# Kernel tuning notes

Measured on AMD Instinct MI355X. Metric: run time of the kernel, lower is better.

## Reference

```python
import math
import jax, jax.numpy as jnp
import numpy as np

NLAT, NLON = 61, 120
C, H = 64, 4
DH = C // H
HID = 128
NSEG = NLAT * NLON  # number of grid points / softmax segments
EPS = 1e-6
SCALE = 1.0 / math.sqrt(DH)


def _build_geometry():
    """Neighbor pairs within theta_cutoff on the equiangular (pole-including) grid.

    The neighborhood structure is longitude-shift invariant, so we enumerate it
    for output longitude 0 and replicate with a modular longitude shift.
    """
    nlat, nlon = NLAT, NLON
    theta = np.pi * np.arange(nlat) / (nlat - 1)           # colatitudes incl. poles
    lam = 2.0 * np.pi * np.arange(nlon) / nlon
    theta_cutoff = 7.0 / math.sqrt(math.pi) * math.pi / (nlat - 1)
    ct, st = np.cos(theta), np.sin(theta)
    # great-circle distance between (theta_o, 0) and (theta_i, dlon): [nlat, nlat, nlon]
    cosd = (ct[:, None, None] * ct[None, :, None]
            + st[:, None, None] * st[None, :, None] * np.cos(lam)[None, None, :])
    dist = np.arccos(np.clip(cosd, -1.0, 1.0))
    ho, hi, dl = np.nonzero(dist <= theta_cutoff)          # E reference-column entries
    wo = np.arange(nlon)
    out_idx = (ho[:, None] * nlon + wo[None, :]).reshape(-1).astype(np.int32)
    in_idx = (hi[:, None] * nlon + (dl[:, None] + wo[None, :]) % nlon).reshape(-1).astype(np.int32)
    # quadrature (integration) weights: sin(theta) measure, zero at the poles
    w = (st * (np.pi / (nlat - 1)) * (2.0 * np.pi / nlon)).astype(np.float32)
    quad_w = np.repeat(w, nlon)                            # [NSEG]
    return jnp.asarray(out_idx), jnp.asarray(in_idx), jnp.asarray(quad_w)


def setup_inputs() -> dict:
    key = jax.random.key(0)
    ks = jax.random.split(key, 8)
    out_idx, in_idx, quad_w = _build_geometry()

    def w(k, shape, fan_in):
        return jax.random.normal(k, shape, dtype=jnp.float32) / np.float32(np.sqrt(fan_in))

    return {
        "x": jax.random.normal(ks[0], (1, C, NLAT, NLON), dtype=jnp.float32),
        "wq": w(ks[1], (C, C), C),
        "wk": w(ks[2], (C, C), C),
        "wv": w(ks[3], (C, C), C),
        "wo": w(ks[4], (C, C), C),
        "w1": w(ks[5], (HID, C), C),
        "b1": jnp.zeros((HID,), jnp.float32),
        "w2": w(ks[6], (C, HID), HID),
        "b2": jnp.zeros((C,), jnp.float32),
        "ln0_g": jnp.ones((C,), jnp.float32),
        "ln0_b": jnp.zeros((C,), jnp.float32),
        "ln1_g": jnp.ones((C,), jnp.float32),
        "ln1_b": jnp.zeros((C,), jnp.float32),
        "quad_w": quad_w,
        "out_idx": out_idx,
        "in_idx": in_idx,
    }


def _layernorm(x, g, b):
    # channel-wise LayerNorm at every spatial location; x: [B, C, H, W]
    m = jnp.mean(x, axis=1, keepdims=True)
    v = jnp.mean((x - m) ** 2, axis=1, keepdims=True)
    xh = (x - m) * jax.lax.rsqrt(v + EPS)
    return xh * g[None, :, None, None] + b[None, :, None, None]


def _neighborhood_attn(x, wq, wk, wv, wo, quad_w, out_idx, in_idx):
    # x: [B, C, nlat, nlon] (fp32)
    B = x.shape[0]
    q = jnp.einsum('oc,bchw->bohw', wq, x).reshape(B, H, DH, NSEG)
    k = jnp.einsum('oc,bchw->bohw', wk, x).reshape(B, H, DH, NSEG)
    v = jnp.einsum('oc,bchw->bohw', wv, x).reshape(B, H, DH, NSEG)
    qg = q[..., out_idx]                                   # [B,H,DH,NNZ]
    kg = k[..., in_idx]
    s = jnp.einsum('bhdn,bhdn->bhn', qg, kg) * SCALE       # [B,H,NNZ]
    s = jnp.moveaxis(s, -1, 0)                             # [NNZ,B,H]
    smax = jax.ops.segment_max(s, out_idx, num_segments=NSEG)
    # quadrature-weighted, numerically stable softmax over each neighborhood
    alpha = jnp.exp(s - smax[out_idx]) * quad_w[in_idx][:, None, None]
    vg = jnp.moveaxis(v[..., in_idx], -1, 0)               # [NNZ,B,H,DH]
    num = jax.ops.segment_sum(alpha[..., None] * vg, out_idx, num_segments=NSEG)
    den = jax.ops.segment_sum(alpha, out_idx, num_segments=NSEG)
    att = num / den[..., None]                             # [NSEG,B,H,DH]
    att = jnp.moveaxis(att, 0, -1).reshape(B, C, NLAT, NLON)
    return jnp.einsum('oc,bchw->bohw', wo, att)


def reference(x, wq, wk, wv, wo, w1, b1, w2, b2, ln0_g, ln0_b, ln1_g, ln1_b,
              quad_w, out_idx, in_idx):
    residual = x
    h0 = _layernorm(x, ln0_g, ln0_b)
    a = _neighborhood_attn(h0.astype(jnp.float32), wq, wk, wv, wo,
                           quad_w, out_idx, in_idx).astype(x.dtype)
    x1 = a + residual
    h1 = _layernorm(x1, ln1_g, ln1_b)
    m = jax.nn.gelu(jnp.einsum('fc,bchw->bfhw', w1, h1) + b1[None, :, None, None],
                    approximate=False)
    m = jnp.einsum('cf,bfhw->bchw', w2, m) + b2[None, :, None, None]
    return m + x1
```

## Files before the change

kernel.cpp:

```cpp
#include <hip/hip_runtime.h>
#include <math.h>

#define NSEG 7320
#define NLON 120
#define HIDN 128
#define ECH  16
#define MAXCH 48

__global__ __launch_bounds__(64) void k1_ln_qkv(
    const float* __restrict__ x,  const float* __restrict__ wq,
    const float* __restrict__ wk, const float* __restrict__ wv,
    const float* __restrict__ g,  const float* __restrict__ b,
    const int* __restrict__ out_idx, const int* __restrict__ in_idx,
    const float* __restrict__ qw, int E,
    float* __restrict__ q_pl, float* __restrict__ k_pl, float* __restrict__ v_pl,
    int* __restrict__ row_start, int4* __restrict__ meta,
    float4* __restrict__ zbase)
{
    const int lane = threadIdx.x;
    const int tile = blockIdx.x;
    const int grp  = blockIdx.y;

    if (grp >= 25) {
        const int n4 = (68 * NSEG) / 4;
        for (int i = ((grp - 25) * 115 + tile) * 64 + lane; i < n4; i += 2 * 115 * 64)
            zbase[i] = make_float4(0.f, 0.f, 0.f, 0.f);
        return;
    }
    if (grp == 24) {
        for (int e = tile * 64 + lane; e < E; e += 115 * 64) {
            int ho = out_idx[e * NLON] / NLON;
            if (e == 0) {
                row_start[ho] = 0;
            } else {
                int hp = out_idx[(e - 1) * NLON] / NLON;
                if (hp != ho) row_start[ho] = e;
            }
            if (e == E - 1) row_start[ho + 1] = E;
            int i0 = in_idx[e * NLON];
            int hi = i0 / NLON;
            int dl = i0 - hi * NLON;
            meta[e] = make_int4(hi * NLON, dl, __float_as_int(qw[i0]), ho);
        }
        return;
    }

    const int n = tile * 64 + lane;
    if (n >= NSEG) return;

    float xv[64];
    float s = 0.f, s2 = 0.f;
#pragma unroll
    for (int c = 0; c < 64; ++c) { float t = x[c * NSEG + n]; xv[c] = t; s += t; s2 += t * t; }
    float mean = s * 0.015625f;
    float var  = s2 * 0.015625f - mean * mean;
    float rstd = rsqrtf(var + 1e-6f);
#pragma unroll
    for (int c = 0; c < 64; ++c) xv[c] = (xv[c] - mean) * rstd * g[c] + b[c];

    const int mm    = grp >> 3;
    const int obase = (grp & 7) * 8;
    const float* __restrict__ w = (mm == 0) ? wq : (mm == 1) ? wk : wv;
    float* __restrict__ dst = (mm == 0) ? q_pl : (mm == 1) ? k_pl : v_pl;
    const float scale = (mm == 0) ? 0.25f : 1.0f;

#pragma unroll
    for (int j = 0; j < 8; ++j) {
        int o = obase + j;
        float acc = 0.f;
#pragma unroll
        for (int c = 0; c < 64; ++c) acc += w[o * 64 + c] * xv[c];
        dst[o * NSEG + n] = acc * scale;
    }
}

__global__ __launch_bounds__(128) void k2_attn(
    const float* __restrict__ q_pl, const float* __restrict__ k_pl,
    const float* __restrict__ v_pl,
    const int4* __restrict__ meta,  const int* __restrict__ row_start,
    float* __restrict__ num, float* __restrict__ den)
{
    const int wo  = threadIdx.x;
    const bool aw = wo < NLON;
    const int woc = aw ? wo : (NLON - 1);
    const int ho  = blockIdx.x;
    const int head = blockIdx.z;
    const int cb  = head * 16;

    int e0 = __builtin_amdgcn_readfirstlane(row_start[ho]);
    int e1 = __builtin_amdgcn_readfirstlane(row_start[ho + 1]);
    int eb = e0 + blockIdx.y * ECH;
    if (eb >= e1) return;
    int ee = eb + ECH; if (ee > e1) ee = e1;

    const int segc = ho * NLON + woc;
    const float* __restrict__ qb = q_pl + (size_t)cb * NSEG;
    const float* __restrict__ kb = k_pl + (size_t)cb * NSEG;
    const float* __restrict__ vb = v_pl + (size_t)cb * NSEG;

    float qreg[16];
#pragma unroll
    for (int c = 0; c < 16; ++c) qreg[c] = qb[c * NSEG + segc];

    float acc[16];
#pragma unroll
    for (int c = 0; c < 16; ++c) acc[c] = 0.f;
    float dh = 0.f;

#pragma unroll 2
    for (int e = eb; e < ee; ++e) {
        int4 mt = meta[e];
        int dlw = mt.y + woc; if (dlw >= NLON) dlw -= NLON;
        const float* __restrict__ kp = kb + (mt.x + dlw);
        const float* __restrict__ vp = vb + (mt.x + dlw);

        float sa = 0.f, sb = 0.f;
#pragma unroll
        for (int c = 0; c < 8; ++c)  sa += qreg[c]     * kp[c * NSEG];
#pragma unroll
        for (int c = 0; c < 8; ++c)  sb += qreg[8 + c] * kp[(8 + c) * NSEG];

        float qwv = aw ? __int_as_float(mt.z) : 0.f;
        float a = __expf(sa + sb) * qwv;
        dh += a;

#pragma unroll
        for (int c = 0; c < 16; ++c) acc[c] = fmaf(a, vp[c * NSEG], acc[c]);
    }

    if (aw) {
        const int seg = ho * NLON + wo;
#pragma unroll
        for (int c = 0; c < 16; ++c) atomicAdd(&num[(cb + c) * NSEG + seg], acc[c]);
        atomicAdd(&den[head * NSEG + seg], dh);
    }
}

__global__ __launch_bounds__(64) void k2c_wo(
    const float* __restrict__ num, const float* __restrict__ den,
    const float* __restrict__ wo,  const float* __restrict__ x,
    float* __restrict__ x1)
{
    const int lane = threadIdx.x;
    const int n    = blockIdx.x * 64 + lane;
    if (n >= NSEG) return;

    float rdh[4];
#pragma unroll
    for (int h = 0; h < 4; ++h) rdh[h] = 1.0f / den[h * NSEG + n];

    float att[64];
#pragma unroll
    for (int c = 0; c < 64; ++c) att[c] = num[c * NSEG + n] * rdh[c >> 4];

    const int o0 = blockIdx.y * 8;
#pragma unroll
    for (int j = 0; j < 8; ++j) {
        int o = o0 + j;
        float acc = 0.f;
#pragma unroll
        for (int c = 0; c < 64; ++c) acc += wo[o * 64 + c] * att[c];
        x1[o * NSEG + n] = acc + x[o * NSEG + n];
    }
}

__global__ __launch_bounds__(64) void k3a_mlp1(
    const float* __restrict__ x1, const float* __restrict__ w1,
    const float* __restrict__ b1, const float* __restrict__ g,
    const float* __restrict__ bb, float* __restrict__ m_act)
{
    const int lane = threadIdx.x;
    const int n    = blockIdx.x * 64 + lane;
    if (n >= NSEG) return;

    float xv[64];
    float s = 0.f, s2 = 0.f;
#pragma unroll
    for (int c = 0; c < 64; ++c) { float t = x1[c * NSEG + n]; xv[c] = t; s += t; s2 += t * t; }
    float mean = s * 0.015625f;
    float var  = s2 * 0.015625f - mean * mean;
    float rstd = rsqrtf(var + 1e-6f);
#pragma unroll
    for (int c = 0; c < 64; ++c) xv[c] = (xv[c] - mean) * rstd * g[c] + bb[c];

    const int h0 = blockIdx.y * 8;
#pragma unroll
    for (int j = 0; j < 8; ++j) {
        int h = h0 + j;
        float mh = b1[h];
#pragma unroll
        for (int c = 0; c < 64; ++c) mh += w1[h * 64 + c] * xv[c];
        m_act[h * NSEG + n] = 0.5f * mh * (1.0f + erff(mh * 0.70710678118654752f));
    }
}

__global__ __launch_bounds__(64) void k3b_mlp2(
    const float* __restrict__ m_act, const float* __restrict__ w2,
    const float* __restrict__ b2,    const float* __restrict__ x1,
    float* __restrict__ out)
{
    const int lane = threadIdx.x;
    const int n    = blockIdx.x * 64 + lane;
    if (n >= NSEG) return;
    const int c0   = blockIdx.y * 8;

    float acc[8];
#pragma unroll
    for (int j = 0; j < 8; ++j) acc[j] = 0.f;

#pragma unroll 8
    for (int h = 0; h < HIDN; ++h) {
        float mh = m_act[h * NSEG + n];
#pragma unroll
        for (int j = 0; j < 8; ++j) acc[j] += w2[(c0 + j) * HIDN + h] * mh;
    }
#pragma unroll
    for (int j = 0; j < 8; ++j) {
        int c = c0 + j;
        out[c * NSEG + n] = acc[j] + b2[c] + x1[c * NSEG + n];
    }
}

extern "C" void kernel_launch(void* const* d_in, const int* in_sizes, int n_in,
                              void* d_out, int out_size, void* d_ws, size_t ws_size,
                              hipStream_t stream)
{
    const float* x    = (const float*)d_in[0];
    const float* wq   = (const float*)d_in[1];
    const float* wk   = (const float*)d_in[2];
    const float* wv   = (const float*)d_in[3];
    const float* wo   = (const float*)d_in[4];
    const float* w1   = (const float*)d_in[5];
    const float* b1   = (const float*)d_in[6];
    const float* w2   = (const float*)d_in[7];
    const float* b2   = (const float*)d_in[8];
    const float* ln0g = (const float*)d_in[9];
    const float* ln0b = (const float*)d_in[10];
    const float* ln1g = (const float*)d_in[11];
    const float* ln1b = (const float*)d_in[12];
    const float* qw   = (const float*)d_in[13];
    const int* out_idx = (const int*)d_in[14];
    const int* in_idx  = (const int*)d_in[15];
    float* out = (float*)d_out;

    const int NNZ = in_sizes[15];
    const int E   = NNZ / NLON;
    const size_t N64 = (size_t)NSEG * 64;

    float* ws    = (float*)d_ws;
    float* q_pl  = ws;
    float* k_pl  = ws + N64;
    float* v_pl  = ws + 2 * N64;
    float* num   = ws + 3 * N64;
    float* den   = ws + 4 * N64;
    float* x1    = ws + 4 * N64 + 4 * NSEG;
    float* m_act = ws + 5 * N64 + 4 * NSEG;
    int*   row_start = (int*)(ws + 7 * N64 + 4 * NSEG);
    int4*  meta  = (int4*)(ws + 7 * N64 + 4 * NSEG + 64);

    hipLaunchKernelGGL(k1_ln_qkv, dim3(115, 27), dim3(64), 0, stream,
                       x, wq, wk, wv, ln0g, ln0b, out_idx, in_idx, qw, E,
                       q_pl, k_pl, v_pl, row_start, meta, (float4*)num);
    hipLaunchKernelGGL(k2_attn, dim3(61, MAXCH, 4), dim3(128), 0, stream,
                       q_pl, k_pl, v_pl, meta, row_start, num, den);
    hipLaunchKernelGGL(k2c_wo, dim3(115, 8), dim3(64), 0, stream,
                       num, den, wo, x, x1);
    hipLaunchKernelGGL(k3a_mlp1, dim3(115, 16), dim3(64), 0, stream,
                       x1, w1, b1, ln1g, ln1b, m_act);
    hipLaunchKernelGGL(k3b_mlp2, dim3(115, 8), dim3(64), 0, stream,
                       m_act, w2, b2, x1, out);
}
```

Measured before the change: 186.8 us.

## Fuse output projection with MLP first layer and flatten attention grid ordering

Merges the Wo projection plus residual kernel with the LayerNorm and first MLP layer kernel. Each block recomputes the full 64-channel x1 in registers, then produces 16 hidden units, and only the first y-block writes x1. This removes one launch and the x1 write-then-read round trip, but the Wo GEMV is now repeated 8 times per point and the larger register arrays may reduce occupancy. The attention kernel grid becomes a 1D launch where consecutive block IDs cover groups of 8 latitude rows for the same head and chunk, which changes scheduling and cache locality, and the id-to-row mapping skips rows at or above 61.

```diff
diff --git a/kernel.cpp b/kernel.cpp
--- a/kernel.cpp
+++ b/kernel.cpp
@@ -80,16 +80,20 @@
     const int4* __restrict__ meta,  const int* __restrict__ row_start,
     float* __restrict__ num, float* __restrict__ den)
 {
+    const int id   = blockIdx.x;
+    const int ho   = (id & 7) + 8 * ((id >> 3) & 7);
+    if (ho >= 61) return;
+    const int ch   = id >> 6;
+    const int head = ch & 3;
+    const int cb   = head * 16;
+
     const int wo  = threadIdx.x;
     const bool aw = wo < NLON;
     const int woc = aw ? wo : (NLON - 1);
-    const int ho  = blockIdx.x;
-    const int head = blockIdx.z;
-    const int cb  = head * 16;
 
     int e0 = __builtin_amdgcn_readfirstlane(row_start[ho]);
     int e1 = __builtin_amdgcn_readfirstlane(row_start[ho + 1]);
-    int eb = e0 + blockIdx.y * ECH;
+    int eb = e0 + (ch >> 2) * ECH;
     if (eb >= e1) return;
     int ee = eb + ECH; if (ee > e1) ee = e1;
 
@@ -136,10 +140,12 @@
     }
 }
 
-__global__ __launch_bounds__(64) void k2c_wo(
+__global__ __launch_bounds__(64) void k23a_wo_mlp1(
     const float* __restrict__ num, const float* __restrict__ den,
     const float* __restrict__ wo,  const float* __restrict__ x,
-    float* __restrict__ x1)
+    const float* __restrict__ w1,  const float* __restrict__ b1,
+    const float* __restrict__ g1,  const float* __restrict__ bb1,
+    float* __restrict__ x1, float* __restrict__ m_act)
 {
     const int lane = threadIdx.x;
     const int n    = blockIdx.x * 64 + lane;
@@ -149,49 +155,43 @@
 #pragma unroll
     for (int h = 0; h < 4; ++h) rdh[h] = 1.0f / den[h * NSEG + n];
 
-    float att[64];
-#pragma unroll
-    for (int c = 0; c < 64; ++c) att[c] = num[c * NSEG + n] * rdh[c >> 4];
-
-    const int o0 = blockIdx.y * 8;
-#pragma unroll
-    for (int j = 0; j < 8; ++j) {
-        int o = o0 + j;
-        float acc = 0.f;
-#pragma unroll
-        for (int c = 0; c < 64; ++c) acc += wo[o * 64 + c] * att[c];
-        x1[o * NSEG + n] = acc + x[o * NSEG + n];
-    }
-}
-
-__global__ __launch_bounds__(64) void k3a_mlp1(
-    const float* __restrict__ x1, const float* __restrict__ w1,
-    const float* __restrict__ b1, const float* __restrict__ g,
-    const float* __restrict__ bb, float* __restrict__ m_act)
-{
-    const int lane = threadIdx.x;
-    const int n    = blockIdx.x * 64 + lane;
-    if (n >= NSEG) return;
-
-    float xv[64];
+    float x1v[64];
+#pragma unroll
+    for (int o = 0; o < 64; ++o) x1v[o] = x[o * NSEG + n];
+
+    for (int c = 0; c < 64; ++c) {
+        float att = num[c * NSEG + n] * rdh[c >> 4];
+        const float* __restrict__ wcol = wo + c;
+#pragma unroll
+        for (int o = 0; o < 64; ++o) x1v[o] = fmaf(wcol[o * 64], att, x1v[o]);
+    }
+
+    if (blockIdx.y == 0) {
+#pragma unroll
+        for (int o = 0; o < 64; ++o) x1[o * NSEG + n] = x1v[o];
+    }
+
     float s = 0.f, s2 = 0.f;
 #pragma unroll
-    for (int c = 0; c < 64; ++c) { float t = x1[c * NSEG + n]; xv[c] = t; s += t; s2 += t * t; }
+    for (int o = 0; o < 64; ++o) { s += x1v[o]; s2 += x1v[o] * x1v[o]; }
     float mean = s * 0.015625f;
     float var  = s2 * 0.015625f - mean * mean;
     float rstd = rsqrtf(var + 1e-6f);
-#pragma unroll
-    for (int c = 0; c < 64; ++c) xv[c] = (xv[c] - mean) * rstd * g[c] + bb[c];
-
-    const int h0 = blockIdx.y * 8;
-#pragma unroll
-    for (int j = 0; j < 8; ++j) {
-        int h = h0 + j;
-        float mh = b1[h];
-#pragma unroll
-        for (int c = 0; c < 64; ++c) mh += w1[h * 64 + c] * xv[c];
-        m_act[h * NSEG + n] = 0.5f * mh * (1.0f + erff(mh * 0.70710678118654752f));
-    }
+
+    const int h0 = blockIdx.y * 16;
+    float mh[16];
+#pragma unroll
+    for (int j = 0; j < 16; ++j) mh[j] = b1[h0 + j];
+    for (int c = 0; c < 64; ++c) {
+        float xn = (x1v[c] - mean) * rstd * g1[c] + bb1[c];
+        const float* __restrict__ w1c = w1 + h0 * 64 + c;
+#pragma unroll
+        for (int j = 0; j < 16; ++j) mh[j] = fmaf(w1c[j * 64], xn, mh[j]);
+    }
+#pragma unroll
+    for (int j = 0; j < 16; ++j)
+        m_act[(h0 + j) * NSEG + n] =
+            0.5f * mh[j] * (1.0f + erff(mh[j] * 0.70710678118654752f));
 }
 
 __global__ __launch_bounds__(64) void k3b_mlp2(
@@ -261,12 +261,10 @@
     hipLaunchKernelGGL(k1_ln_qkv, dim3(115, 27), dim3(64), 0, stream,
                        x, wq, wk, wv, ln0g, ln0b, out_idx, in_idx, qw, E,
                        q_pl, k_pl, v_pl, row_start, meta, (float4*)num);
-    hipLaunchKernelGGL(k2_attn, dim3(61, MAXCH, 4), dim3(128), 0, stream,
+    hipLaunchKernelGGL(k2_attn, dim3(64 * 192), dim3(128), 0, stream,
                        q_pl, k_pl, v_pl, meta, row_start, num, den);
-    hipLaunchKernelGGL(k2c_wo, dim3(115, 8), dim3(64), 0, stream,
-                       num, den, wo, x, x1);
-    hipLaunchKernelGGL(k3a_mlp1, dim3(115, 16), dim3(64), 0, stream,
-                       x1, w1, b1, ln1g, ln1b, m_act);
+    hipLaunchKernelGGL(k23a_wo_mlp1, dim3(115, 8), dim3(64), 0, stream,
+                       num, den, wo, x, w1, b1, ln1g, ln1b, x1, m_act);
     hipLaunchKernelGGL(k3b_mlp2, dim3(115, 8), dim3(64), 0, stream,
                        m_act, w2, b2, x1, out);
 }
```

Result: slower. 227.2 us (+21.6%).

## Replace atomic edge-chunk attention with per-row block LDS reduction

Applied to the files above, without the earlier changes.

The attention kernel now uses one 512-thread block per (latitude row, head). Four sub-groups stride over the row's neighbor entries and reduce through shared memory, replacing chunked blocks that accumulated with global atomics. This removes the zeroing pass in the first kernel and the atomic traffic. The cost is far fewer blocks (244) with serial per-row work, which risks poor occupancy on a large GPU and load imbalance across rows of different neighborhood sizes. The MLP1 kernel also computes 16 hidden units per thread instead of 8, halving its grid.

```diff
diff --git a/kernel.cpp b/kernel.cpp
--- a/kernel.cpp
+++ b/kernel.cpp
@@ -4,8 +4,6 @@
 #define NSEG 7320
 #define NLON 120
 #define HIDN 128
-#define ECH  16
-#define MAXCH 48
 
 __global__ __launch_bounds__(64) void k1_ln_qkv(
     const float* __restrict__ x,  const float* __restrict__ wq,
@@ -14,19 +12,12 @@
     const int* __restrict__ out_idx, const int* __restrict__ in_idx,
     const float* __restrict__ qw, int E,
     float* __restrict__ q_pl, float* __restrict__ k_pl, float* __restrict__ v_pl,
-    int* __restrict__ row_start, int4* __restrict__ meta,
-    float4* __restrict__ zbase)
+    int* __restrict__ row_start, int4* __restrict__ meta)
 {
     const int lane = threadIdx.x;
     const int tile = blockIdx.x;
     const int grp  = blockIdx.y;
 
-    if (grp >= 25) {
-        const int n4 = (68 * NSEG) / 4;
-        for (int i = ((grp - 25) * 115 + tile) * 64 + lane; i < n4; i += 2 * 115 * 64)
-            zbase[i] = make_float4(0.f, 0.f, 0.f, 0.f);
-        return;
-    }
     if (grp == 24) {
         for (int e = tile * 64 + lane; e < E; e += 115 * 64) {
             int ho = out_idx[e * NLON] / NLON;
@@ -74,24 +65,25 @@
     }
 }
 
-__global__ __launch_bounds__(128) void k2_attn(
+__global__ __launch_bounds__(512) void k2_attn(
     const float* __restrict__ q_pl, const float* __restrict__ k_pl,
     const float* __restrict__ v_pl,
     const int4* __restrict__ meta,  const int* __restrict__ row_start,
     float* __restrict__ num, float* __restrict__ den)
 {
-    const int wo  = threadIdx.x;
-    const bool aw = wo < NLON;
-    const int woc = aw ? wo : (NLON - 1);
-    const int ho  = blockIdx.x;
-    const int head = blockIdx.z;
-    const int cb  = head * 16;
+    __shared__ float lds[4][17][128];
+
+    const int tid = threadIdx.x;
+    const int sub = tid >> 7;
+    const int wol = tid & 127;
+    const bool aw = wol < NLON;
+    const int woc = aw ? wol : (NLON - 1);
+    const int ho   = blockIdx.x;
+    const int head = blockIdx.y;
+    const int cb   = head * 16;
 
     int e0 = __builtin_amdgcn_readfirstlane(row_start[ho]);
     int e1 = __builtin_amdgcn_readfirstlane(row_start[ho + 1]);
-    int eb = e0 + blockIdx.y * ECH;
-    if (eb >= e1) return;
-    int ee = eb + ECH; if (ee > e1) ee = e1;
 
     const int segc = ho * NLON + woc;
     const float* __restrict__ qb = q_pl + (size_t)cb * NSEG;
@@ -108,7 +100,7 @@
     float dh = 0.f;
 
 #pragma unroll 2
-    for (int e = eb; e < ee; ++e) {
+    for (int e = e0 + sub; e < e1; e += 4) {
         int4 mt = meta[e];
         int dlw = mt.y + woc; if (dlw >= NLON) dlw -= NLON;
         const float* __restrict__ kp = kb + (mt.x + dlw);
@@ -128,11 +120,21 @@
         for (int c = 0; c < 16; ++c) acc[c] = fmaf(a, vp[c * NSEG], acc[c]);
     }
 
-    if (aw) {
-        const int seg = ho * NLON + wo;
-#pragma unroll
-        for (int c = 0; c < 16; ++c) atomicAdd(&num[(cb + c) * NSEG + seg], acc[c]);
-        atomicAdd(&den[head * NSEG + seg], dh);
+#pragma unroll
+    for (int c = 0; c < 16; ++c) lds[sub][c][wol] = acc[c];
+    lds[sub][16][wol] = dh;
+    __syncthreads();
+
+    if (sub == 0 && aw) {
+        const int seg = ho * NLON + wol;
+#pragma unroll
+        for (int c = 0; c < 16; ++c) {
+            float sm = lds[0][c][wol] + lds[1][c][wol]
+                     + lds[2][c][wol] + lds[3][c][wol];
+            num[(cb + c) * NSEG + seg] = sm;
+        }
+        den[head * NSEG + seg] = lds[0][16][wol] + lds[1][16][wol]
+                               + lds[2][16][wol] + lds[3][16][wol];
     }
 }
 
@@ -183,9 +185,9 @@
 #pragma unroll
     for (int c = 0; c < 64; ++c) xv[c] = (xv[c] - mean) * rstd * g[c] + bb[c];
 
-    const int h0 = blockIdx.y * 8;
-#pragma unroll
-    for (int j = 0; j < 8; ++j) {
+    const int h0 = blockIdx.y * 16;
+#pragma unroll
+    for (int j = 0; j < 16; ++j) {
         int h = h0 + j;
         float mh = b1[h];
 #pragma unroll
@@ -258,14 +260,14 @@
     int*   row_start = (int*)(ws + 7 * N64 + 4 * NSEG);
     int4*  meta  = (int4*)(ws + 7 * N64 + 4 * NSEG + 64);
 
-    hipLaunchKernelGGL(k1_ln_qkv, dim3(115, 27), dim3(64), 0, stream,
+    hipLaunchKernelGGL(k1_ln_qkv, dim3(115, 25), dim3(64), 0, stream,
                        x, wq, wk, wv, ln0g, ln0b, out_idx, in_idx, qw, E,
-                       q_pl, k_pl, v_pl, row_start, meta, (float4*)num);
-    hipLaunchKernelGGL(k2_attn, dim3(61, MAXCH, 4), dim3(128), 0, stream,
+                       q_pl, k_pl, v_pl, row_start, meta);
+    hipLaunchKernelGGL(k2_attn, dim3(61, 4), dim3(512), 0, stream,
                        q_pl, k_pl, v_pl, meta, row_start, num, den);
     hipLaunchKernelGGL(k2c_wo, dim3(115, 8), dim3(64), 0, stream,
                        num, den, wo, x, x1);
-    hipLaunchKernelGGL(k3a_mlp1, dim3(115, 16), dim3(64), 0, stream,
+    hipLaunchKernelGGL(k3a_mlp1, dim3(115, 8), dim3(64), 0, stream,
                        x1, w1, b1, ln1g, ln1b, m_act);
     hipLaunchKernelGGL(k3b_mlp2, dim3(115, 8), dim3(64), 0, stream,
                        m_act, w2, b2, x1, out);
```

Result: slower. 259.5 us (+38.9%).

## Replace attention atomics with per-chunk partial buffers reduced in output projection

Applied to the files above, without the earlier changes.

The attention kernel no longer accumulates numerator and denominator with global atomicAdd. Each edge chunk now writes its partial sums to its own slice of a partial buffer, and the output-projection kernel sums the chunks for each row before normalising. This removes atomic contention and the zero-fill pass that used to run in the first kernel. In exchange the partial buffer is much larger (up to 48 chunks × 68 × NSEG), and k2c_wo now reads many more values per point in a non-unrolled loop, which adds memory traffic.

```diff
diff --git a/kernel.cpp b/kernel.cpp
--- a/kernel.cpp
+++ b/kernel.cpp
@@ -14,19 +14,12 @@
     const int* __restrict__ out_idx, const int* __restrict__ in_idx,
     const float* __restrict__ qw, int E,
     float* __restrict__ q_pl, float* __restrict__ k_pl, float* __restrict__ v_pl,
-    int* __restrict__ row_start, int4* __restrict__ meta,
-    float4* __restrict__ zbase)
+    int* __restrict__ row_start, int4* __restrict__ meta)
 {
     const int lane = threadIdx.x;
     const int tile = blockIdx.x;
     const int grp  = blockIdx.y;
 
-    if (grp >= 25) {
-        const int n4 = (68 * NSEG) / 4;
-        for (int i = ((grp - 25) * 115 + tile) * 64 + lane; i < n4; i += 2 * 115 * 64)
-            zbase[i] = make_float4(0.f, 0.f, 0.f, 0.f);
-        return;
-    }
     if (grp == 24) {
         for (int e = tile * 64 + lane; e < E; e += 115 * 64) {
             int ho = out_idx[e * NLON] / NLON;
@@ -78,18 +71,19 @@
     const float* __restrict__ q_pl, const float* __restrict__ k_pl,
     const float* __restrict__ v_pl,
     const int4* __restrict__ meta,  const int* __restrict__ row_start,
-    float* __restrict__ num, float* __restrict__ den)
+    float* __restrict__ part)
 {
     const int wo  = threadIdx.x;
     const bool aw = wo < NLON;
     const int woc = aw ? wo : (NLON - 1);
     const int ho  = blockIdx.x;
+    const int j   = blockIdx.y;
     const int head = blockIdx.z;
     const int cb  = head * 16;
 
     int e0 = __builtin_amdgcn_readfirstlane(row_start[ho]);
     int e1 = __builtin_amdgcn_readfirstlane(row_start[ho + 1]);
-    int eb = e0 + blockIdx.y * ECH;
+    int eb = e0 + j * ECH;
     if (eb >= e1) return;
     int ee = eb + ECH; if (ee > e1) ee = e1;
 
@@ -130,38 +124,53 @@
 
     if (aw) {
         const int seg = ho * NLON + wo;
-#pragma unroll
-        for (int c = 0; c < 16; ++c) atomicAdd(&num[(cb + c) * NSEG + seg], acc[c]);
-        atomicAdd(&den[head * NSEG + seg], dh);
+        float* __restrict__ pb = part + ((size_t)j * 68) * NSEG;
+#pragma unroll
+        for (int c = 0; c < 16; ++c)
+            pb[(cb + c) * NSEG + seg] = acc[c];
+        pb[(64 + head) * NSEG + seg] = dh;
     }
 }
 
 __global__ __launch_bounds__(64) void k2c_wo(
-    const float* __restrict__ num, const float* __restrict__ den,
-    const float* __restrict__ wo,  const float* __restrict__ x,
+    const float* __restrict__ part, const int* __restrict__ row_start,
+    const float* __restrict__ wo,   const float* __restrict__ x,
     float* __restrict__ x1)
 {
     const int lane = threadIdx.x;
     const int n    = blockIdx.x * 64 + lane;
     if (n >= NSEG) return;
-
+    const int row  = n / NLON;
+    const int len  = row_start[row + 1] - row_start[row];
+    const int nch  = (len + ECH - 1) / ECH;
+
+    float den[4] = {0.f, 0.f, 0.f, 0.f};
+    for (int j = 0; j < nch; ++j) {
+        const float* __restrict__ pb = part + ((size_t)j * 68 + 64) * NSEG + n;
+#pragma unroll
+        for (int h = 0; h < 4; ++h) den[h] += pb[h * NSEG];
+    }
     float rdh[4];
 #pragma unroll
-    for (int h = 0; h < 4; ++h) rdh[h] = 1.0f / den[h * NSEG + n];
-
-    float att[64];
-#pragma unroll
-    for (int c = 0; c < 64; ++c) att[c] = num[c * NSEG + n] * rdh[c >> 4];
+    for (int h = 0; h < 4; ++h) rdh[h] = 1.0f / den[h];
 
     const int o0 = blockIdx.y * 8;
-#pragma unroll
-    for (int j = 0; j < 8; ++j) {
-        int o = o0 + j;
-        float acc = 0.f;
-#pragma unroll
-        for (int c = 0; c < 64; ++c) acc += wo[o * 64 + c] * att[c];
-        x1[o * NSEG + n] = acc + x[o * NSEG + n];
-    }
+    float acc[8];
+#pragma unroll
+    for (int j = 0; j < 8; ++j) acc[j] = 0.f;
+
+    for (int c = 0; c < 64; ++c) {
+        float s = 0.f;
+        for (int j = 0; j < nch; ++j)
+            s += part[((size_t)j * 68 + c) * NSEG + n];
+        s *= rdh[c >> 4];
+        const float* __restrict__ wc = wo + o0 * 64 + c;
+#pragma unroll
+        for (int o = 0; o < 8; ++o) acc[o] = fmaf(wc[o * 64], s, acc[o]);
+    }
+#pragma unroll
+    for (int o = 0; o < 8; ++o)
+        x1[(o0 + o) * NSEG + n] = acc[o] + x[(o0 + o) * NSEG + n];
 }
 
 __global__ __launch_bounds__(64) void k3a_mlp1(
@@ -251,20 +260,19 @@
     float* q_pl  = ws;
     float* k_pl  = ws + N64;
     float* v_pl  = ws + 2 * N64;
-    float* num   = ws + 3 * N64;
-    float* den   = ws + 4 * N64;
-    float* x1    = ws + 4 * N64 + 4 * NSEG;
-    float* m_act = ws + 5 * N64 + 4 * NSEG;
-    int*   row_start = (int*)(ws + 7 * N64 + 4 * NSEG);
-    int4*  meta  = (int4*)(ws + 7 * N64 + 4 * NSEG + 64);
-
-    hipLaunchKernelGGL(k1_ln_qkv, dim3(115, 27), dim3(64), 0, stream,
+    float* x1    = ws + 3 * N64;
+    float* m_act = ws + 4 * N64;
+    int*   row_start = (int*)(ws + 6 * N64);
+    int4*  meta  = (int4*)(ws + 6 * N64 + 64);
+    float* part  = ws + 6 * N64 + 64 + 4 * 10240;
+
+    hipLaunchKernelGGL(k1_ln_qkv, dim3(115, 25), dim3(64), 0, stream,
                        x, wq, wk, wv, ln0g, ln0b, out_idx, in_idx, qw, E,
-                       q_pl, k_pl, v_pl, row_start, meta, (float4*)num);
+                       q_pl, k_pl, v_pl, row_start, meta);
     hipLaunchKernelGGL(k2_attn, dim3(61, MAXCH, 4), dim3(128), 0, stream,
-                       q_pl, k_pl, v_pl, meta, row_start, num, den);
+                       q_pl, k_pl, v_pl, meta, row_start, part);
     hipLaunchKernelGGL(k2c_wo, dim3(115, 8), dim3(64), 0, stream,
-                       num, den, wo, x, x1);
+                       part, row_start, wo, x, x1);
     hipLaunchKernelGGL(k3a_mlp1, dim3(115, 16), dim3(64), 0, stream,
                        x1, w1, b1, ln1g, ln1b, m_act);
     hipLaunchKernelGGL(k3b_mlp2, dim3(115, 8), dim3(64), 0, stream,
```

Result: slower. 691.3 us (+270.1%).
